# Kernel optimization log

Hardware: AMD Instinct MI355X
Metric: run time of the kernel (lower is better)

The kernel has to match this reference:

```python
import jax, jax.numpy as jnp
import numpy as np
from jax import lax

WIN = 7            # skimage default win_size
K1, K2 = 0.01, 0.03
DATA_RANGE = 1.0


def _uniform_filter_valid(x):
    # (skimage uses reflect-padded uniform_filter then crops pad=3, which equals
    #  a valid windowed mean.)
    c, h, w = x.shape
    x4 = x[:, None]                                   # (C,1,H,W)
    kh = jnp.full((1, 1, WIN, 1), 1.0 / WIN, x.dtype)
    kw = jnp.full((1, 1, 1, WIN), 1.0 / WIN, x.dtype)
    dn = ('NCHW', 'OIHW', 'NCHW')
    x4 = lax.conv_general_dilated(x4, kh, (1, 1), 'VALID', dimension_numbers=dn)
    x4 = lax.conv_general_dilated(x4, kw, (1, 1), 'VALID', dimension_numbers=dn)
    return x4[:, 0]


def setup_inputs() -> dict:
    key = jax.random.key(0)
    k1, k2 = jax.random.split(key)
    shape = (32, 3, 512, 512)
    return {
        'input_tensor': jax.random.uniform(k1, shape, dtype=jnp.float32),
        'target': jax.random.uniform(k2, shape, dtype=jnp.float32),
    }


def reference(input_tensor, target):
    h, w = input_tensor.shape[-2:]
    x = input_tensor.reshape(-1, h, w).astype(jnp.float32)
    y = target.reshape(-1, h, w).astype(jnp.float32)

    C1 = (K1 * DATA_RANGE) ** 2
    C2 = (K2 * DATA_RANGE) ** 2
    NP = WIN * WIN
    cov_norm = NP / (NP - 1.0)  # sample covariance (skimage default)

    ux = _uniform_filter_valid(x)
    uy = _uniform_filter_valid(y)
    uxx = _uniform_filter_valid(x * x)
    uyy = _uniform_filter_valid(y * y)
    uxy = _uniform_filter_valid(x * y)

    vx = cov_norm * (uxx - ux * ux)
    vy = cov_norm * (uyy - uy * uy)
    vxy = cov_norm * (uxy - ux * uy)

    S = ((2.0 * ux * uy + C1) * (2.0 * vxy + C2)) / (
        (ux * ux + uy * uy + C1) * (vx + vy + C2))
    # mean over cropped spatial map per channel, then over channels == global mean
    return jnp.mean(S)
```

## Files before the change

### kernel.cpp

```cpp
#include <hip/hip_runtime.h>


namespace {
constexpr int W      = 512;
constexpr int HH     = 512;
constexpr int NIMG   = 96;
constexpr int OW     = 506;
constexpr int RSTRIP = 23;
constexpr int NSTRIP = 22;
constexpr float C1f   = 1.0e-4f;
constexpr float C2f   = 9.0e-4f;
constexpr float COVN  = 49.0f / 48.0f;
constexpr float INV49 = 1.0f / 49.0f;
constexpr double NPIX = 96.0 * 506.0 * 506.0;
constexpr int LSTRIDE = 520;
}

__global__ __launch_bounds__(256) void ssim_main(const float* __restrict__ X,
                                                 const float* __restrict__ Y,
                                                 double* __restrict__ acc)
{
    __shared__ float ldsV[5 * LSTRIDE];
    __shared__ float wsum[4];

    const int t   = threadIdx.x;
    const int c   = t * 2;
    const int img = blockIdx.y;
    const int r0  = blockIdx.x * RSTRIP;

    const float* xb = X + (size_t)img * W * HH;
    const float* yb = Y + (size_t)img * W * HH;

    float V[5][2];
#pragma unroll
    for (int q = 0; q < 5; q++)
#pragma unroll
        for (int i = 0; i < 2; i++) V[q][i] = 0.0f;

#pragma unroll
    for (int k = 0; k < 6; k++) {
        float2 x2 = *(const float2*)(xb + (size_t)(r0 + k) * W + c);
        float2 y2 = *(const float2*)(yb + (size_t)(r0 + k) * W + c);
        float xs[2] = {x2.x, x2.y};
        float ys[2] = {y2.x, y2.y};
#pragma unroll
        for (int i = 0; i < 2; i++) {
            V[0][i] += xs[i];
            V[1][i] += ys[i];
            V[2][i] = fmaf(xs[i], xs[i], V[2][i]);
            V[3][i] = fmaf(ys[i], ys[i], V[3][i]);
            V[4][i] = fmaf(xs[i], ys[i], V[4][i]);
        }
    }

    float2 xn = *(const float2*)(xb + (size_t)(r0 + 6) * W + c);
    float2 yn = *(const float2*)(yb + (size_t)(r0 + 6) * W + c);

    float sacc = 0.0f;

    for (int j = 0; j < RSTRIP; j++) {
        {
            float xs[2] = {xn.x, xn.y};
            float ys[2] = {yn.x, yn.y};
#pragma unroll
            for (int i = 0; i < 2; i++) {
                V[0][i] += xs[i];
                V[1][i] += ys[i];
                V[2][i] = fmaf(xs[i], xs[i], V[2][i]);
                V[3][i] = fmaf(ys[i], ys[i], V[3][i]);
                V[4][i] = fmaf(xs[i], ys[i], V[4][i]);
            }
        }

#pragma unroll
        for (int q = 0; q < 5; q++) {
            *(float2*)&ldsV[q * LSTRIDE + c] = make_float2(V[q][0], V[q][1]);
        }

        float2 xo = *(const float2*)(xb + (size_t)(r0 + j) * W + c);
        float2 yo = *(const float2*)(yb + (size_t)(r0 + j) * W + c);
        int rn = r0 + j + 7; if (rn > HH - 1) rn = HH - 1;
        float2 xn2 = *(const float2*)(xb + (size_t)rn * W + c);
        float2 yn2 = *(const float2*)(yb + (size_t)rn * W + c);

        __syncthreads();

        float Hs[5][2];
#pragma unroll
        for (int q = 0; q < 5; q++) {
            const float* P = &ldsV[q * LSTRIDE];
            float2 n1 = *(const float2*)(P + c + 2);
            float2 n2 = *(const float2*)(P + c + 4);
            float2 n3 = *(const float2*)(P + c + 6);
            float v0 = V[q][0], v1 = V[q][1];
            float h0 = ((v0 + v1) + (n1.x + n1.y)) + ((n2.x + n2.y) + n3.x);
            float h1 = h0 - v0 + n3.y;
            Hs[q][0] = h0; Hs[q][1] = h1;
        }

        __syncthreads();

#pragma unroll
        for (int i = 0; i < 2; i++) {
            float ux  = Hs[0][i] * INV49;
            float uy  = Hs[1][i] * INV49;
            float uxx = Hs[2][i] * INV49;
            float uyy = Hs[3][i] * INV49;
            float uxy = Hs[4][i] * INV49;
            float uxuy = ux * uy;
            float a1 = fmaf(2.0f, uxuy, C1f);
            float b1 = fmaf(ux, ux, fmaf(uy, uy, C1f));
            float vxy = COVN * (uxy - uxuy);
            float a2 = fmaf(2.0f, vxy, C2f);
            float vs  = COVN * ((uxx - ux * ux) + (uyy - uy * uy));
            float b2 = vs + C2f;
            float S = (a1 * a2) / (b1 * b2);
            if (c + i < OW) sacc += S;
        }

        {
            float xs[2] = {xo.x, xo.y};
            float ys[2] = {yo.x, yo.y};
#pragma unroll
            for (int i = 0; i < 2; i++) {
                V[0][i] -= xs[i];
                V[1][i] -= ys[i];
                V[2][i] = fmaf(-xs[i], xs[i], V[2][i]);
                V[3][i] = fmaf(-ys[i], ys[i], V[3][i]);
                V[4][i] = fmaf(-xs[i], ys[i], V[4][i]);
            }
        }
        xn = xn2; yn = yn2;
    }

#pragma unroll
    for (int off = 32; off > 0; off >>= 1)
        sacc += __shfl_down(sacc, off);
    if ((t & 63) == 0) wsum[t >> 6] = sacc;
    __syncthreads();
    if (t == 0) atomicAdd(acc, (double)((wsum[0] + wsum[1]) + (wsum[2] + wsum[3])));
}

__global__ void ssim_finalize(const double* __restrict__ acc, float* __restrict__ out)
{
    out[0] = (float)(acc[0] / NPIX);
}

extern "C" void kernel_launch(void* const* d_in, const int* in_sizes, int n_in,
                              void* d_out, int out_size, void* d_ws, size_t ws_size,
                              hipStream_t stream)
{
    const float* X = (const float*)d_in[0];
    const float* Y = (const float*)d_in[1];
    float* out = (float*)d_out;
    double* acc = (double*)d_ws;

    hipMemsetAsync(d_ws, 0, sizeof(double), stream);
    ssim_main<<<dim3(NSTRIP, NIMG), 256, 0, stream>>>(X, Y, acc);
    ssim_finalize<<<1, 1, 0, stream>>>(acc, out);
}
```

Baseline: 236.6 us.

## Replace LDS horizontal sum with wave shuffles over overlapping column segments

Each block now uses five wavefronts, and each wave owns a 122-column segment that overlaps its neighbour, so the horizontal 7-tap sum can be built from in-wave __shfl_down calls. This removes the LDS staging and the two __syncthreads per output row. The SSIM formula is rewritten on raw window sums with folded constants and a hardware reciprocal in place of the division. The cost is some redundant loads at segment overlaps, 25% more threads, and slightly lower precision from rcp.

```diff
diff --git a/kernel.cpp b/kernel.cpp
--- a/kernel.cpp
+++ b/kernel.cpp
@@ -8,28 +8,37 @@
 constexpr int OW     = 506;
 constexpr int RSTRIP = 23;
 constexpr int NSTRIP = 22;
-constexpr float C1f   = 1.0e-4f;
-constexpr float C2f   = 9.0e-4f;
-constexpr float COVN  = 49.0f / 48.0f;
-constexpr float INV49 = 1.0f / 49.0f;
-constexpr double NPIX = 96.0 * 506.0 * 506.0;
-constexpr int LSTRIDE = 520;
+constexpr int SEGW   = 122;
+constexpr float D1      = 0.2401f;
+constexpr float D2      = 2.1609f;
+constexpr float COVN    = 49.0f / 48.0f;
+constexpr float COV2    = 2.0f * COVN;
+constexpr float K49COV  = 49.0f * COVN;
+constexpr float K49COV2 = 2.0f * 49.0f * COVN;
+constexpr double NPIX   = 96.0 * 506.0 * 506.0;
 }
 
-__global__ __launch_bounds__(256) void ssim_main(const float* __restrict__ X,
-                                                 const float* __restrict__ Y,
-                                                 double* __restrict__ acc)
+__global__ __launch_bounds__(320, 6) void ssim_main(const float* __restrict__ X,
+                                                    const float* __restrict__ Y,
+                                                    double* __restrict__ acc)
 {
-    __shared__ float ldsV[5 * LSTRIDE];
-    __shared__ float wsum[4];
+    __shared__ float wsum[5];
 
-    const int t   = threadIdx.x;
-    const int c   = t * 2;
-    const int img = blockIdx.y;
-    const int r0  = blockIdx.x * RSTRIP;
+    const int t    = threadIdx.x;
+    const int wave = t >> 6;
+    const int lane = t & 63;
+    const int img  = blockIdx.y;
+    const int r0   = blockIdx.x * RSTRIP;
 
-    const float* xb = X + (size_t)img * W * HH;
-    const float* yb = Y + (size_t)img * W * HH;
+    const int s  = wave * SEGW;
+    const int lc = 2 * lane;
+    int g = s + lc; if (g > W - 2) g = W - 2;
+
+    const float* xb = X + (size_t)img * W * HH + g;
+    const float* yb = Y + (size_t)img * W * HH + g;
+
+    const bool ok0 = (lc     < SEGW) && (s + lc     < OW);
+    const bool ok1 = (lc + 1 < SEGW) && (s + lc + 1 < OW);
 
     float V[5][2];
 #pragma unroll
@@ -39,8 +48,8 @@
 
 #pragma unroll
     for (int k = 0; k < 6; k++) {
-        float2 x2 = *(const float2*)(xb + (size_t)(r0 + k) * W + c);
-        float2 y2 = *(const float2*)(yb + (size_t)(r0 + k) * W + c);
+        float2 x2 = *(const float2*)(xb + (size_t)(r0 + k) * W);
+        float2 y2 = *(const float2*)(yb + (size_t)(r0 + k) * W);
         float xs[2] = {x2.x, x2.y};
         float ys[2] = {y2.x, y2.y};
 #pragma unroll
@@ -53,8 +62,8 @@
         }
     }
 
-    float2 xn = *(const float2*)(xb + (size_t)(r0 + 6) * W + c);
-    float2 yn = *(const float2*)(yb + (size_t)(r0 + 6) * W + c);
+    float2 xn = *(const float2*)(xb + (size_t)(r0 + 6) * W);
+    float2 yn = *(const float2*)(yb + (size_t)(r0 + 6) * W);
 
     float sacc = 0.0f;
 
@@ -72,50 +81,39 @@
             }
         }
 
-#pragma unroll
-        for (int q = 0; q < 5; q++) {
-            *(float2*)&ldsV[q * LSTRIDE + c] = make_float2(V[q][0], V[q][1]);
-        }
-
-        float2 xo = *(const float2*)(xb + (size_t)(r0 + j) * W + c);
-        float2 yo = *(const float2*)(yb + (size_t)(r0 + j) * W + c);
+        float2 xo  = *(const float2*)(xb + (size_t)(r0 + j) * W);
+        float2 yo  = *(const float2*)(yb + (size_t)(r0 + j) * W);
         int rn = r0 + j + 7; if (rn > HH - 1) rn = HH - 1;
-        float2 xn2 = *(const float2*)(xb + (size_t)rn * W + c);
-        float2 yn2 = *(const float2*)(yb + (size_t)rn * W + c);
-
-        __syncthreads();
+        float2 xn2 = *(const float2*)(xb + (size_t)rn * W);
+        float2 yn2 = *(const float2*)(yb + (size_t)rn * W);
 
         float Hs[5][2];
 #pragma unroll
         for (int q = 0; q < 5; q++) {
-            const float* P = &ldsV[q * LSTRIDE];
-            float2 n1 = *(const float2*)(P + c + 2);
-            float2 n2 = *(const float2*)(P + c + 4);
-            float2 n3 = *(const float2*)(P + c + 6);
             float v0 = V[q][0], v1 = V[q][1];
-            float h0 = ((v0 + v1) + (n1.x + n1.y)) + ((n2.x + n2.y) + n3.x);
-            float h1 = h0 - v0 + n3.y;
-            Hs[q][0] = h0; Hs[q][1] = h1;
+            float P  = v0 + v1;
+            float P1 = __shfl_down(P,  1);
+            float P2 = __shfl_down(P,  2);
+            float P3 = __shfl_down(P,  3);
+            float a3 = __shfl_down(v0, 3);
+            Hs[q][0] = (P  + P1) + (P2 + a3);
+            Hs[q][1] = (v1 + P1) + (P2 + P3);
         }
-
-        __syncthreads();
 
 #pragma unroll
         for (int i = 0; i < 2; i++) {
-            float ux  = Hs[0][i] * INV49;
-            float uy  = Hs[1][i] * INV49;
-            float uxx = Hs[2][i] * INV49;
-            float uyy = Hs[3][i] * INV49;
-            float uxy = Hs[4][i] * INV49;
-            float uxuy = ux * uy;
-            float a1 = fmaf(2.0f, uxuy, C1f);
-            float b1 = fmaf(ux, ux, fmaf(uy, uy, C1f));
-            float vxy = COVN * (uxy - uxuy);
-            float a2 = fmaf(2.0f, vxy, C2f);
-            float vs  = COVN * ((uxx - ux * ux) + (uyy - uy * uy));
-            float b2 = vs + C2f;
-            float S = (a1 * a2) / (b1 * b2);
-            if (c + i < OW) sacc += S;
+            float U0 = Hs[0][i], U1 = Hs[1][i];
+            float U2 = Hs[2][i], U3 = Hs[3][i], U4 = Hs[4][i];
+            float A    = U0 * U1;
+            float q01  = fmaf(U0, U0, U1 * U1);
+            float num1 = fmaf(2.0f, A, D1);
+            float den1 = q01 + D1;
+            float num2 = fmaf(K49COV2, U4, fmaf(-COV2, A, D2));
+            float s23  = U2 + U3;
+            float den2 = fmaf(K49COV, s23, fmaf(-COVN, q01, D2));
+            float S = (num1 * num2) * __builtin_amdgcn_rcpf(den1 * den2);
+            bool ok = i ? ok1 : ok0;
+            sacc += ok ? S : 0.0f;
         }
 
         {
@@ -136,9 +134,12 @@
 #pragma unroll
     for (int off = 32; off > 0; off >>= 1)
         sacc += __shfl_down(sacc, off);
-    if ((t & 63) == 0) wsum[t >> 6] = sacc;
+    if (lane == 0) wsum[wave] = sacc;
     __syncthreads();
-    if (t == 0) atomicAdd(acc, (double)((wsum[0] + wsum[1]) + (wsum[2] + wsum[3])));
+    if (t == 0) {
+        float b = ((wsum[0] + wsum[1]) + (wsum[2] + wsum[3])) + wsum[4];
+        atomicAdd(acc, (double)b);
+    }
 }
 
 __global__ void ssim_finalize(const double* __restrict__ acc, float* __restrict__ out)
@@ -156,6 +157,6 @@
     double* acc = (double*)d_ws;
 
     hipMemsetAsync(d_ws, 0, sizeof(double), stream);
-    ssim_main<<<dim3(NSTRIP, NIMG), 256, 0, stream>>>(X, Y, acc);
+    ssim_main<<<dim3(NSTRIP, NIMG), 320, 0, stream>>>(X, Y, acc);
     ssim_finalize<<<1, 1, 0, stream>>>(acc, out);
 }
```

Result: slower. 243.6 us (+2.9%).
